# Performance work log

Hardware: AMD Instinct MI355X
Metric: run time of the kernel (lower is better)

## Reference

```python
import jax, jax.numpy as jnp
import numpy as np

B, L, D = 1, 2048, 512
NL, N, K = 4, 16, 4
DI = 2 * D          # mamba expand=2
R = D // 16         # dt_rank = ceil(D/16)
H = 4 * D           # mlp hidden


def _ln(x, w, b, eps=1e-5):
    mu = x.mean(-1, keepdims=True)
    v = ((x - mu) ** 2).mean(-1, keepdims=True)
    return (x - mu) * jax.lax.rsqrt(v + eps) * w + b


def _rms(x, w, eps=1e-5):
    return x * jax.lax.rsqrt((x * x).mean(-1, keepdims=True) + eps) * w


def _ssm_scan(delta, Bm, Cm, u, A, Dp):
    # delta,u: (B,L,DI); Bm,Cm: (B,L,N); A: (DI,N); Dp: (DI,)
    def step(h, inp):
        d_t, b_t, c_t, u_t = inp                              # (B,DI),(B,N),(B,N),(B,DI)
        dA = jnp.exp(d_t[..., None] * A)                      # (B,DI,N)
        h = dA * h + (d_t * u_t)[..., None] * b_t[:, None, :]
        y = jnp.einsum('bdn,bn->bd', h, c_t)
        return h, y
    h0 = jnp.zeros((delta.shape[0], DI, N), delta.dtype)
    xs = (delta.swapaxes(0, 1), Bm.swapaxes(0, 1), Cm.swapaxes(0, 1), u.swapaxes(0, 1))
    _, ys = jax.lax.scan(step, h0, xs)
    return ys.swapaxes(0, 1) + u * Dp


def _mamba(h, in_w, cw, cb, xw, dtw, dtb, A_log, Dp, ow):
    xz = h @ in_w.T                                           # (B,L,2*DI)
    x, z = jnp.split(xz, 2, axis=-1)
    # causal depthwise conv1d, kernel K, left pad K-1
    xp = jnp.pad(x, ((0, 0), (K - 1, 0), (0, 0)))
    Ls = x.shape[1]
    x = sum(cw[:, k] * xp[:, k:k + Ls, :] for k in range(K)) + cb
    x = jax.nn.silu(x)
    dbc = x @ xw.T                                            # (B,L,R+2N)
    dt, Bm, Cm = dbc[..., :R], dbc[..., R:R + N], dbc[..., R + N:]
    delta = jax.nn.softplus(dt @ dtw.T + dtb)                 # (B,L,DI)
    A = -jnp.exp(A_log)                                       # (DI,N)
    y = _ssm_scan(delta, Bm, Cm, x, A, Dp)
    y = y * jax.nn.silu(z)
    return y @ ow.T


def _forward(hidden_states, ln1_w, ln1_b, in_proj_w, conv_w, conv_b, x_proj_w,
             dt_proj_w, dt_proj_b, A_log, D_param, out_proj_w, block_norm_w,
             norm_f_w, ln2_w, ln2_b, fc1_w, fc1_b, fc2_w, fc2_b):
    shortcut = hidden_states
    h = _ln(hidden_states, ln1_w, ln1_b)
    residual = None
    for i in range(in_proj_w.shape[0]):
        residual = h if residual is None else h + residual    # residual_in_fp32
        hn = _rms(residual, block_norm_w[i])                  # fused_add_norm prenorm
        h = _mamba(hn, in_proj_w[i], conv_w[i], conv_b[i], x_proj_w[i],
                   dt_proj_w[i], dt_proj_b[i], A_log[i], D_param[i], out_proj_w[i])
    h = _rms(h + residual, norm_f_w)                          # final rms_norm_fn
    h = shortcut + h
    x = _ln(h, ln2_w, ln2_b)
    x = jax.nn.gelu(x @ fc1_w.T + fc1_b)
    x = x @ fc2_w.T + fc2_b
    return h + x


def setup_inputs() -> dict:
    key = jax.random.key(0)
    ks = jax.random.split(key, 9)
    s = 0.02
    return {
        'hidden_states': jax.random.normal(ks[0], (B, L, D), jnp.float32),
        'ln1_w': jnp.ones((D,), jnp.float32),
        'ln1_b': jnp.zeros((D,), jnp.float32),
        'in_proj_w': jax.random.normal(ks[1], (NL, 2 * DI, D), jnp.float32) * s,
        'conv_w': jax.random.normal(ks[2], (NL, DI, K), jnp.float32) * 0.3,
        'conv_b': jnp.zeros((NL, DI), jnp.float32),
        'x_proj_w': jax.random.normal(ks[3], (NL, R + 2 * N, DI), jnp.float32) * s,
        'dt_proj_w': jax.random.normal(ks[4], (NL, DI, R), jnp.float32) * s,
        'dt_proj_b': jax.random.uniform(ks[5], (NL, DI), jnp.float32, -4.0, -2.0),
        'A_log': jnp.tile(jnp.log(jnp.arange(1, N + 1, dtype=jnp.float32)), (NL, DI, 1)),
        'D_param': jnp.ones((NL, DI), jnp.float32),
        'out_proj_w': jax.random.normal(ks[6], (NL, D, DI), jnp.float32) * s,
        'block_norm_w': jnp.ones((NL, D), jnp.float32),
        'norm_f_w': jnp.ones((D,), jnp.float32),
        'ln2_w': jnp.ones((D,), jnp.float32),
        'ln2_b': jnp.zeros((D,), jnp.float32),
        'fc1_w': jax.random.normal(ks[7], (H, D), jnp.float32) * s,
        'fc1_b': jnp.zeros((H,), jnp.float32),
        'fc2_w': jax.random.normal(ks[8], (D, H), jnp.float32) * s,
        'fc2_b': jnp.zeros((D,), jnp.float32),
    }


def reference(hidden_states, ln1_w, ln1_b, in_proj_w, conv_w, conv_b, x_proj_w,
              dt_proj_w, dt_proj_b, A_log, D_param, out_proj_w, block_norm_w,
              norm_f_w, ln2_w, ln2_b, fc1_w, fc1_b, fc2_w, fc2_b):
    return _forward(hidden_states, ln1_w, ln1_b, in_proj_w, conv_w, conv_b,
                    x_proj_w, dt_proj_w, dt_proj_b, A_log, D_param, out_proj_w,
                    block_norm_w, norm_f_w, ln2_w, ln2_b, fc1_w, fc1_b, fc2_w, fc2_b)
```

## Files before the change

kernel.cpp:

```cpp
#include <hip/hip_runtime.h>
#include <hip/hip_bf16.h>
#include <math.h>

#define L_SEQ 2048
#define Dm    512
#define DI    1024
#define Nst   16
#define Kc    4
#define Rr    32
#define NL    4
#define CH    128
#define LC    (L_SEQ / CH)
#define KSX   8

typedef __attribute__((ext_vector_type(8))) short bf16x8;
typedef __attribute__((ext_vector_type(4))) float f32x4;

__device__ __forceinline__ float act_softplus(float x) {
    return fmaxf(x, 0.f) + log1pf(__expf(-fabsf(x)));
}
__device__ __forceinline__ float act_gelu(float x) {
    float c = 0.7978845608028654f * (x + 0.044715f * x * x * x);
    float t = 1.f - 2.f / (__expf(2.f * c) + 1.f);
    return 0.5f * x * (1.f + t);
}
__device__ __forceinline__ float silu_(float x) {
    return x / (1.f + __expf(-x));
}
__device__ __forceinline__ ushort f2bf(float f) {
    union { float f; unsigned u; } c; c.f = f;
    unsigned r = c.u + 0x7fffu + ((c.u >> 16) & 1u);
    return (ushort)(r >> 16);
}
__device__ __forceinline__ float bf2f(ushort u) {
    union { unsigned u; float f; } c; c.u = ((unsigned)u) << 16;
    return c.f;
}
__device__ __forceinline__ float wave_sum(float v) {
    #pragma unroll
    for (int off = 32; off; off >>= 1) v += __shfl_xor(v, off);
    return v;
}

__global__ __launch_bounds__(256) void setup_kernel(
    const float* __restrict__ s0, ushort* __restrict__ d0, int n0,
    const float* __restrict__ s1, ushort* __restrict__ d1, int n1,
    const float* __restrict__ s2, ushort* __restrict__ d2, int n2,
    const float* __restrict__ s3, ushort* __restrict__ d3, int n3,
    const float* __restrict__ s4, ushort* __restrict__ d4, int n4_,
    const float* __restrict__ s5, ushort* __restrict__ d5, int n5,
    const float* __restrict__ x, const float* __restrict__ w,
    const float* __restrict__ b, const float* __restrict__ rw,
    float* __restrict__ res, ushort* __restrict__ hn_bf)
{
    if (blockIdx.x < 512) {
        int lane = threadIdx.x & 63, wv = threadIdx.x >> 6;
        int row = blockIdx.x * 4 + wv;
        size_t base = (size_t)row * Dm + lane * 8;
        float v[8];
        *(float4*)(v)     = *(const float4*)(x + base);
        *(float4*)(v + 4) = *(const float4*)(x + base + 4);
        float s = 0.f, ss = 0.f;
        #pragma unroll
        for (int q = 0; q < 8; ++q) { s += v[q]; ss += v[q] * v[q]; }
        s = wave_sum(s); ss = wave_sum(ss);
        float mu = s * (1.f / Dm);
        float rs = rsqrtf(ss * (1.f / Dm) - mu * mu + 1e-5f);
        float wv8[8], bv8[8], rv8[8];
        *(float4*)(wv8)     = *(const float4*)(w + lane * 8);
        *(float4*)(wv8 + 4) = *(const float4*)(w + lane * 8 + 4);
        *(float4*)(bv8)     = *(const float4*)(b + lane * 8);
        *(float4*)(bv8 + 4) = *(const float4*)(b + lane * 8 + 4);
        *(float4*)(rv8)     = *(const float4*)(rw + lane * 8);
        *(float4*)(rv8 + 4) = *(const float4*)(rw + lane * 8 + 4);
        float o[8], ss2 = 0.f;
        #pragma unroll
        for (int q = 0; q < 8; ++q) {
            o[q] = (v[q] - mu) * rs * wv8[q] + bv8[q];
            ss2 += o[q] * o[q];
        }
        *(float4*)(res + base)     = *(float4*)(o);
        *(float4*)(res + base + 4) = *(float4*)(o + 4);
        ss2 = wave_sum(ss2);
        float rr = rsqrtf(ss2 * (1.f / Dm) + 1e-5f);
        bf16x8 hb;
        #pragma unroll
        for (int q = 0; q < 8; ++q) hb[q] = (short)f2bf(o[q] * rr * rv8[q]);
        *(bf16x8*)(hn_bf + base) = hb;
        return;
    }
    int i = (blockIdx.x - 512) * 256 + threadIdx.x;
    const float* s; ushort* d;
    if (i < n0) { s = s0; d = d0; }
    else { i -= n0; if (i < n1) { s = s1; d = d1; }
    else { i -= n1; if (i < n2) { s = s2; d = d2; }
    else { i -= n2; if (i < n3) { s = s3; d = d3; }
    else { i -= n3; if (i < n4_) { s = s4; d = d4; }
    else { i -= n4_; if (i < n5) { s = s5; d = d5; } else return; } } } } }
    float4 v = ((const float4*)s)[i];
    ushort4 o;
    o.x = f2bf(v.x); o.y = f2bf(v.y); o.z = f2bf(v.z); o.w = f2bf(v.w);
    ((ushort4*)d)[i] = o;
}

__global__ __launch_bounds__(256) void add_rms_kernel(const ushort* __restrict__ hb,
    float* __restrict__ res, const float* __restrict__ w, ushort* __restrict__ rms_out)
{
    int lane = threadIdx.x & 63, wv = threadIdx.x >> 6;
    int row = blockIdx.x * 4 + wv;
    size_t base = (size_t)row * Dm + lane * 8;
    bf16x8 hv = *(const bf16x8*)(hb + base);
    float v[8];
    *(float4*)(v)     = *(const float4*)(res + base);
    *(float4*)(v + 4) = *(const float4*)(res + base + 4);
    float ss = 0.f;
    #pragma unroll
    for (int q = 0; q < 8; ++q) {
        v[q] += bf2f((ushort)hv[q]);
        ss += v[q] * v[q];
    }
    *(float4*)(res + base)     = *(float4*)(v);
    *(float4*)(res + base + 4) = *(float4*)(v + 4);
    ss = wave_sum(ss);
    float rr = rsqrtf(ss * (1.f / Dm) + 1e-5f);
    float wv8[8];
    *(float4*)(wv8)     = *(const float4*)(w + lane * 8);
    *(float4*)(wv8 + 4) = *(const float4*)(w + lane * 8 + 4);
    bf16x8 ob;
    #pragma unroll
    for (int q = 0; q < 8; ++q) ob[q] = (short)f2bf(v[q] * rr * wv8[q]);
    *(bf16x8*)(rms_out + base) = ob;
}

__global__ __launch_bounds__(256) void final_ln2_kernel(const ushort* __restrict__ hb,
    const float* __restrict__ res, const float* __restrict__ shortcut,
    const float* __restrict__ wf, const float* __restrict__ w2,
    const float* __restrict__ b2, float* __restrict__ hout,
    ushort* __restrict__ yb16)
{
    int lane = threadIdx.x & 63, wv = threadIdx.x >> 6;
    int row = blockIdx.x * 4 + wv;
    size_t base = (size_t)row * Dm + lane * 8;
    bf16x8 hv = *(const bf16x8*)(hb + base);
    float v[8];
    *(float4*)(v)     = *(const float4*)(res + base);
    *(float4*)(v + 4) = *(const float4*)(res + base + 4);
    float ss = 0.f;
    #pragma unroll
    for (int q = 0; q < 8; ++q) {
        v[q] += bf2f((ushort)hv[q]);
        ss += v[q] * v[q];
    }
    ss = wave_sum(ss);
    float rs = rsqrtf(ss * (1.f / Dm) + 1e-5f);
    float sc[8], wf8[8];
    *(float4*)(sc)     = *(const float4*)(shortcut + base);
    *(float4*)(sc + 4) = *(const float4*)(shortcut + base + 4);
    *(float4*)(wf8)     = *(const float4*)(wf + lane * 8);
    *(float4*)(wf8 + 4) = *(const float4*)(wf + lane * 8 + 4);
    float t[8], s2 = 0.f, ss2 = 0.f;
    #pragma unroll
    for (int q = 0; q < 8; ++q) {
        t[q] = sc[q] + v[q] * rs * wf8[q];
        s2 += t[q]; ss2 += t[q] * t[q];
    }
    *(float4*)(hout + base)     = *(float4*)(t);
    *(float4*)(hout + base + 4) = *(float4*)(t + 4);
    s2 = wave_sum(s2); ss2 = wave_sum(ss2);
    float mu = s2 * (1.f / Dm);
    float rsig = rsqrtf(ss2 * (1.f / Dm) - mu * mu + 1e-5f);
    float w28[8], b28[8];
    *(float4*)(w28)     = *(const float4*)(w2 + lane * 8);
    *(float4*)(w28 + 4) = *(const float4*)(w2 + lane * 8 + 4);
    *(float4*)(b28)     = *(const float4*)(b2 + lane * 8);
    *(float4*)(b28 + 4) = *(const float4*)(b2 + lane * 8 + 4);
    bf16x8 ob;
    #pragma unroll
    for (int q = 0; q < 8; ++q) ob[q] = (short)f2bf((t[q] - mu) * rsig * w28[q] + b28[q]);
    *(bf16x8*)(yb16 + base) = ob;
}

template<int BM, int BN, int BK, int EPI>
__global__ __launch_bounds__(256) void gemm_mfma(
    const ushort* __restrict__ A, int lda,
    const ushort* __restrict__ W, int K,
    void* __restrict__ Cout, int ldc,
    const float* __restrict__ bias, const float* __restrict__ addsrc)
{
    constexpr int ROWB  = BK * 2;
    constexpr int SMASK = (ROWB / 16) - 1;
    constexpr int KK    = BK / 32;
    constexpr int WM = BM / 2, WN = BN / 2;
    constexpr int FM = WM / 16, FN = WN / 16;
    constexpr int ISS_A = (BM * ROWB) / 4096;
    constexpr int ISS_W = (BN * ROWB) / 4096;

    __shared__ __align__(16) ushort As[BM * BK];
    __shared__ __align__(16) ushort Ws[BN * BK];

    int tid = threadIdx.x;
    int wave = tid >> 6, lane = tid & 63;
    int wr = wave >> 1, wc = wave & 1;
    int l16 = lane & 15, lk = lane >> 4;
    int bm = blockIdx.y * BM, bn = blockIdx.x * BN;

    const ushort* srcA[ISS_A];
    const ushort* srcW[ISS_W];
    #pragma unroll
    for (int s = 0; s < ISS_A; ++s) {
        int off = s * 4096 + wave * 1024 + lane * 16;
        int row = off / ROWB;
        int slot = (off % ROWB) >> 4;
        int col = ((slot ^ (row & SMASK)) << 3);
        srcA[s] = A + (size_t)(bm + row) * lda + col;
    }
    #pragma unroll
    for (int s = 0; s < ISS_W; ++s) {
        int off = s * 4096 + wave * 1024 + lane * 16;
        int row = off / ROWB;
        int slot = (off % ROWB) >> 4;
        int col = ((slot ^ (row & SMASK)) << 3);
        srcW[s] = W + (size_t)(bn + row) * K + col;
    }
    int aoff[FM][KK], woff[FN][KK];
    #pragma unroll
    for (int i = 0; i < FM; ++i) {
        int row = wr * WM + i * 16 + l16;
        #pragma unroll
        for (int kk = 0; kk < KK; ++kk)
            aoff[i][kk] = row * BK + ((((kk << 2) | lk) ^ (row & SMASK)) << 3);
    }
    #pragma unroll
    for (int j = 0; j < FN; ++j) {
        int row = wc * WN + j * 16 + l16;
        #pragma unroll
        for (int kk = 0; kk < KK; ++kk)
            woff[j][kk] = row * BK + ((((kk << 2) | lk) ^ (row & SMASK)) << 3);
    }

    f32x4 acc[FM][FN] = {};

    for (int k0 = 0; k0 < K; k0 += BK) {
        #pragma unroll
        for (int s = 0; s < ISS_A; ++s)
            __builtin_amdgcn_global_load_lds(
                (const __attribute__((address_space(1))) void*)(srcA[s] + k0),
                (__attribute__((address_space(3))) void*)((char*)As + s * 4096 + wave * 1024),
                16, 0, 0);
        #pragma unroll
        for (int s = 0; s < ISS_W; ++s)
            __builtin_amdgcn_global_load_lds(
                (const __attribute__((address_space(1))) void*)(srcW[s] + k0),
                (__attribute__((address_space(3))) void*)((char*)Ws + s * 4096 + wave * 1024),
                16, 0, 0);
        __syncthreads();
        #pragma unroll
        for (int kk = 0; kk < KK; ++kk) {
            bf16x8 af[FM], wf[FN];
            #pragma unroll
            for (int i = 0; i < FM; ++i) af[i] = *(const bf16x8*)(As + aoff[i][kk]);
            #pragma unroll
            for (int j = 0; j < FN; ++j) wf[j] = *(const bf16x8*)(Ws + woff[j][kk]);
            #pragma unroll
            for (int i = 0; i < FM; ++i)
                #pragma unroll
                for (int j = 0; j < FN; ++j)
                    acc[i][j] = __builtin_amdgcn_mfma_f32_16x16x32_bf16(af[i], wf[j], acc[i][j], 0, 0, 0);
        }
        __syncthreads();
    }

    int orow0 = bm + wr * WM, ocol0 = bn + wc * WN;
    #pragma unroll
    for (int j = 0; j < FN; ++j) {
        int col = ocol0 + j * 16 + l16;
        float bj = 0.f;
        if constexpr (EPI == 2 || EPI == 4) bj = bias[col];
        #pragma unroll
        for (int i = 0; i < FM; ++i) {
            #pragma unroll
            for (int r = 0; r < 4; ++r) {
                int row = orow0 + i * 16 + lk * 4 + r;
                float v = acc[i][j][r];
                if constexpr (EPI == 1) {
                    ((ushort*)Cout)[(size_t)row * ldc + col] = f2bf(v);
                } else if constexpr (EPI == 2) {
                    ((ushort*)Cout)[(size_t)row * ldc + col] = f2bf(act_gelu(v + bj));
                } else if constexpr (EPI == 4) {
                    ((float*)Cout)[(size_t)row * ldc + col] = v + bj + addsrc[(size_t)row * ldc + col];
                }
            }
        }
    }
}

__global__ __launch_bounds__(256) void xproj_conv_kernel(
    const ushort* __restrict__ xz, const float* __restrict__ cw,
    const float* __restrict__ cb, const ushort* __restrict__ W,
    ushort* __restrict__ xc, float* __restrict__ part)
{
    constexpr int BM = 64, BN = 64, BK = 64;
    constexpr int ROWB  = BK * 2;
    constexpr int SMASK = (ROWB / 16) - 1;
    constexpr int KK    = BK / 32;
    constexpr int WM = 32, WN = 32, FM = 2, FN = 2;

    __shared__ __align__(16) ushort As[BM * BK];
    __shared__ __align__(16) ushort Ws[BN * BK];

    int tid = threadIdx.x;
    int wave = tid >> 6, lane = tid & 63;
    int wr = wave >> 1, wc = wave & 1;
    int l16 = lane & 15, lk = lane >> 4;
    int bm = blockIdx.y * BM;
    int z = blockIdx.z;
    int kbeg = z * (DI / KSX);

    const ushort* srcW[2];
    #pragma unroll
    for (int s = 0; s < 2; ++s) {
        int off = s * 4096 + wave * 1024 + lane * 16;
        int row = off / ROWB;
        int slot = (off % ROWB) >> 4;
        int col = ((slot ^ (row & SMASK)) << 3);
        srcW[s] = W + (size_t)row * DI + kbeg + col;
    }
    int aoff[FM][KK], woff[FN][KK];
    #pragma unroll
    for (int i = 0; i < FM; ++i) {
        int row = wr * WM + i * 16 + l16;
        #pragma unroll
        for (int kk = 0; kk < KK; ++kk)
            aoff[i][kk] = row * BK + ((((kk << 2) | lk) ^ (row & SMASK)) << 3);
    }
    #pragma unroll
    for (int j = 0; j < FN; ++j) {
        int row = wc * WN + j * 16 + l16;
        #pragma unroll
        for (int kk = 0; kk < KK; ++kk)
            woff[j][kk] = row * BK + ((((kk << 2) | lk) ^ (row & SMASK)) << 3);
    }

    f32x4 acc[FM][FN] = {};

    for (int k0 = 0; k0 < DI / KSX; k0 += BK) {
        #pragma unroll
        for (int s = 0; s < 2; ++s)
            __builtin_amdgcn_global_load_lds(
                (const __attribute__((address_space(1))) void*)(srcW[s] + k0),
                (__attribute__((address_space(3))) void*)((char*)Ws + s * 4096 + wave * 1024),
                16, 0, 0);
        #pragma unroll
        for (int s = 0; s < 2; ++s) {
            int off = s * 4096 + wave * 1024 + lane * 16;
            int row = off >> 7;
            int slot = (off >> 4) & 7;
            int t = bm + row;
            int dcol = kbeg + k0 + slot * 8;
            float a[8];
            float4 c4[8];
            #pragma unroll
            for (int q = 0; q < 8; ++q) {
                a[q] = cb[dcol + q];
                c4[q] = *(const float4*)(cw + (size_t)(dcol + q) * 4);
            }
            #pragma unroll
            for (int k = 0; k < 4; ++k) {
                int tt = t + k - 3;
                if (tt >= 0) {
                    bf16x8 xv = *(const bf16x8*)(xz + (size_t)tt * (2 * DI) + dcol);
                    #pragma unroll
                    for (int q = 0; q < 8; ++q) {
                        float wk = (k == 0) ? c4[q].x : (k == 1) ? c4[q].y
                                 : (k == 2) ? c4[q].z : c4[q].w;
                        a[q] = fmaf(wk, bf2f((ushort)xv[q]), a[q]);
                    }
                }
            }
            bf16x8 o;
            #pragma unroll
            for (int q = 0; q < 8; ++q) o[q] = (short)f2bf(silu_(a[q]));
            *(bf16x8*)(xc + (size_t)t * DI + dcol) = o;
            *(bf16x8*)(As + row * BK + ((slot ^ (row & SMASK)) << 3)) = o;
        }
        __syncthreads();
        #pragma unroll
        for (int kk = 0; kk < KK; ++kk) {
            bf16x8 af[FM], wf[FN];
            #pragma unroll
            for (int i = 0; i < FM; ++i) af[i] = *(const bf16x8*)(As + aoff[i][kk]);
            #pragma unroll
            for (int j = 0; j < FN; ++j) wf[j] = *(const bf16x8*)(Ws + woff[j][kk]);
            #pragma unroll
            for (int i = 0; i < FM; ++i)
                #pragma unroll
                for (int j = 0; j < FN; ++j)
                    acc[i][j] = __builtin_amdgcn_mfma_f32_16x16x32_bf16(af[i], wf[j], acc[i][j], 0, 0, 0);
        }
        __syncthreads();
    }

    float* coutf = part + (size_t)z * L_SEQ * 64;
    int orow0 = bm + wr * WM, ocol0 = wc * WN;
    #pragma unroll
    for (int j = 0; j < FN; ++j) {
        int col = ocol0 + j * 16 + l16;
        #pragma unroll
        for (int i = 0; i < FM; ++i)
            #pragma unroll
            for (int r = 0; r < 4; ++r) {
                int row = orow0 + i * 16 + lk * 4 + r;
                coutf[(size_t)row * 64 + col] = acc[i][j][r];
            }
    }
}

__global__ __launch_bounds__(256) void scan_chunk_kernel(
    const float* __restrict__ part, const ushort* __restrict__ u,
    const ushort* __restrict__ wdt, const float* __restrict__ dtb,
    const float* __restrict__ A_log,
    float* __restrict__ hend, float* __restrict__ aprod,
    ushort* __restrict__ delta_bf)
{
    __shared__ float sdt[LC][32];
    __shared__ float bsm[LC][16];
    int tid = threadIdx.x;
    int c = blockIdx.x;
    int d = blockIdx.y * 256 + tid;
    int t0 = c * LC;
    const int S = L_SEQ * 64;
    for (int i = tid; i < LC * 48; i += 256) {
        int tt = i / 48, cc = i % 48;
        int idx = (t0 + tt) * 64 + cc;
        float s = 0.f;
        #pragma unroll
        for (int p = 0; p < KSX; ++p) s += part[idx + p * S];
        if (cc < 32) sdt[tt][cc] = s; else bsm[tt][cc - 32] = s;
    }
    bf16x8 wd[4];
    #pragma unroll
    for (int p = 0; p < 4; ++p) wd[p] = *(const bf16x8*)(wdt + (size_t)d * 32 + p * 8);
    float bd = dtb[d];
    float A2[16];
    {
        float a[16];
        #pragma unroll
        for (int q = 0; q < 4; ++q)
            *(float4*)(a + q * 4) = ((const float4*)(A_log + (size_t)d * 16))[q];
        #pragma unroll
        for (int n = 0; n < 16; ++n)
            A2[n] = -__expf(a[n]) * 1.44269504f;
    }
    float h[16], ap[16];
    #pragma unroll
    for (int n = 0; n < 16; ++n) { h[n] = 0.f; ap[n] = 1.f; }
    __syncthreads();
    for (int tt = 0; tt < LC; ++tt) {
        int t = t0 + tt;
        float dtv = bd;
        #pragma unroll
        for (int p = 0; p < 4; ++p)
            #pragma unroll
            for (int e = 0; e < 8; ++e)
                dtv = fmaf(sdt[tt][p * 8 + e], bf2f((ushort)wd[p][e]), dtv);
        ushort dbf = f2bf(act_softplus(dtv));
        delta_bf[(size_t)t * DI + d] = dbf;
        float dt_ = bf2f(dbf);
        float du = dt_ * bf2f(u[(size_t)t * DI + d]);
        #pragma unroll
        for (int n = 0; n < 16; ++n) {
            float dA = exp2f(dt_ * A2[n]);
            h[n] = fmaf(dA, h[n], du * bsm[tt][n]);
            ap[n] *= dA;
        }
    }
    size_t base = ((size_t)c * DI + d) * 16;
    #pragma unroll
    for (int q = 0; q < 4; ++q) {
        ((float4*)(hend + base))[q]  = *(float4*)(h + q * 4);
        ((float4*)(aprod + base))[q] = *(float4*)(ap + q * 4);
    }
}

__global__ __launch_bounds__(64) void chunk_prefix_kernel(
    const float* __restrict__ hend, float* __restrict__ aprod_hin)
{
    int j = blockIdx.x * 64 + threadIdx.x;
    float h = 0.f;
    for (int cg = 0; cg < CH; cg += 8) {
        float ap[8], he[8];
        #pragma unroll
        for (int q = 0; q < 8; ++q) {
            size_t o = (size_t)(cg + q) * (DI * Nst) + j;
            ap[q] = aprod_hin[o]; he[q] = hend[o];
        }
        #pragma unroll
        for (int q = 0; q < 8; ++q) {
            size_t o = (size_t)(cg + q) * (DI * Nst) + j;
            aprod_hin[o] = h;
            h = fmaf(ap[q], h, he[q]);
        }
    }
}

__global__ __launch_bounds__(256) void scan_apply_kernel(
    const float* __restrict__ part, const ushort* __restrict__ delta,
    const ushort* __restrict__ u, const float* __restrict__ A_log,
    const float* __restrict__ Dp, const ushort* __restrict__ xz,
    const float* __restrict__ hin, ushort* __restrict__ y)
{
    __shared__ float bsm[LC][16], csm[LC][16];
    int tid = threadIdx.x;
    int c = blockIdx.x;
    int d = blockIdx.y * 256 + tid;
    int t0 = c * LC;
    const int S = L_SEQ * 64;
    for (int i = tid; i < LC * 32; i += 256) {
        int tt = i >> 5, k = i & 31;
        int idx = (t0 + tt) * 64 + 32 + k;
        float s = 0.f;
        #pragma unroll
        for (int p = 0; p < KSX; ++p) s += part[idx + p * S];
        if (k < 16) bsm[tt][k] = s; else csm[tt][k - 16] = s;
    }
    float A2[16];
    {
        float a[16];
        #pragma unroll
        for (int q = 0; q < 4; ++q)
            *(float4*)(a + q * 4) = ((const float4*)(A_log + (size_t)d * 16))[q];
        #pragma unroll
        for (int n = 0; n < 16; ++n)
            A2[n] = -__expf(a[n]) * 1.44269504f;
    }
    float h[16];
    size_t base = ((size_t)c * DI + d) * 16;
    #pragma unroll
    for (int q = 0; q < 4; ++q)
        *(float4*)(h + q * 4) = ((const float4*)(hin + base))[q];
    float Dval = Dp[d];
    __syncthreads();
    for (int tt = 0; tt < LC; ++tt) {
        int t = t0 + tt;
        float dt_ = bf2f(delta[(size_t)t * DI + d]);
        float u_  = bf2f(u[(size_t)t * DI + d]);
        float du  = dt_ * u_;
        float acc = 0.f;
        #pragma unroll
        for (int n = 0; n < 16; ++n) {
            float dA = exp2f(dt_ * A2[n]);
            h[n] = fmaf(dA, h[n], du * bsm[tt][n]);
            acc = fmaf(h[n], csm[tt][n], acc);
        }
        float zv = bf2f(xz[(size_t)t * (2 * DI) + DI + d]);
        y[(size_t)t * DI + d] = f2bf((acc + u_ * Dval) * silu_(zv));
    }
}

extern "C" void kernel_launch(void* const* d_in, const int* in_sizes, int n_in,
                              void* d_out, int out_size, void* d_ws, size_t ws_size,
                              hipStream_t stream)
{
    const float* hidden     = (const float*)d_in[0];
    const float* ln1_w      = (const float*)d_in[1];
    const float* ln1_b      = (const float*)d_in[2];
    const float* in_proj_w  = (const float*)d_in[3];
    const float* conv_w     = (const float*)d_in[4];
    const float* conv_b     = (const float*)d_in[5];
    const float* x_proj_w   = (const float*)d_in[6];
    const float* dt_proj_w  = (const float*)d_in[7];
    const float* dt_proj_b  = (const float*)d_in[8];
    const float* A_log      = (const float*)d_in[9];
    const float* D_param    = (const float*)d_in[10];
    const float* out_proj_w = (const float*)d_in[11];
    const float* block_norm_w = (const float*)d_in[12];
    const float* norm_f_w   = (const float*)d_in[13];
    const float* ln2_w      = (const float*)d_in[14];
    const float* ln2_b      = (const float*)d_in[15];
    const float* fc1_w      = (const float*)d_in[16];
    const float* fc1_b      = (const float*)d_in[17];
    const float* fc2_w      = (const float*)d_in[18];
    const float* fc2_b      = (const float*)d_in[19];

    char* P = (char*)d_ws;
    auto alloc = [&](size_t bytes) { char* r = P; P += (bytes + 255) & ~(size_t)255; return r; };
    float* hout   = (float*)alloc((size_t)L_SEQ * Dm * 4);
    float* res    = (float*)alloc((size_t)L_SEQ * Dm * 4);
    float* part   = (float*)alloc((size_t)KSX * L_SEQ * 64 * 4);
    float* hend   = (float*)alloc((size_t)CH * DI * Nst * 4);
    float* aprod  = (float*)alloc((size_t)CH * DI * Nst * 4);
    ushort* h_bf  = (ushort*)alloc((size_t)L_SEQ * Dm * 2);
    ushort* delta_bf = (ushort*)alloc((size_t)L_SEQ * DI * 2);
    ushort* hn_bf = (ushort*)alloc((size_t)L_SEQ * Dm * 2);
    ushort* xz_bf = (ushort*)alloc((size_t)L_SEQ * 2 * DI * 2);
    ushort* xc_bf = (ushort*)alloc((size_t)L_SEQ * DI * 2);
    ushort* yb_bf = (ushort*)alloc((size_t)L_SEQ * DI * 2);
    ushort* w_in  = (ushort*)alloc((size_t)NL * 2 * DI * Dm * 2);
    ushort* w_out = (ushort*)alloc((size_t)NL * Dm * DI * 2);
    ushort* w_x   = (ushort*)alloc((size_t)NL * 64 * DI * 2);
    ushort* w_dt  = (ushort*)alloc((size_t)NL * DI * Rr * 2);
    ushort* w_fc1 = (ushort*)alloc((size_t)(4 * Dm) * Dm * 2);
    ushort* w_fc2 = (ushort*)alloc((size_t)Dm * (4 * Dm) * 2);
    float* out  = (float*)d_out;

    {
        int n0 = NL * 2 * DI * Dm / 4, n1 = NL * Dm * DI / 4, n2 = NL * 64 * DI / 4;
        int n3 = NL * DI * Rr / 4, n4_ = 4 * Dm * Dm / 4, n5 = Dm * 4 * Dm / 4;
        int tot = n0 + n1 + n2 + n3 + n4_ + n5;
        int grid = 512 + (tot + 255) / 256;
        setup_kernel<<<grid, 256, 0, stream>>>(
            in_proj_w, w_in, n0, out_proj_w, w_out, n1, x_proj_w, w_x, n2,
            dt_proj_w, w_dt, n3, fc1_w, w_fc1, n4_, fc2_w, w_fc2, n5,
            hidden, ln1_w, ln1_b, block_norm_w, res, hn_bf);
    }

    dim3 gscan(CH, DI / 256);
    for (int i = 0; i < NL; ++i) {
        if (i) add_rms_kernel<<<L_SEQ / 4, 256, 0, stream>>>(h_bf, res,
                                                  block_norm_w + i * Dm, hn_bf);
        gemm_mfma<128, 64, 128, 1><<<dim3(2 * DI / 64, L_SEQ / 128), 256, 0, stream>>>(
            hn_bf, Dm, w_in + (size_t)i * 2 * DI * Dm, Dm, xz_bf, 2 * DI, nullptr, nullptr);
        xproj_conv_kernel<<<dim3(1, L_SEQ / 64, KSX), 256, 0, stream>>>(
            xz_bf, conv_w + i * DI * Kc, conv_b + i * DI,
            w_x + (size_t)i * 64 * DI, xc_bf, part);
        scan_chunk_kernel<<<gscan, 256, 0, stream>>>(part, xc_bf,
                                        w_dt + (size_t)i * DI * Rr, dt_proj_b + i * DI,
                                        A_log + (size_t)i * DI * Nst, hend, aprod, delta_bf);
        chunk_prefix_kernel<<<(DI * Nst) / 64, 64, 0, stream>>>(hend, aprod);
        scan_apply_kernel<<<gscan, 256, 0, stream>>>(part, delta_bf, xc_bf,
                                        A_log + (size_t)i * DI * Nst,
                                        D_param + i * DI, xz_bf, aprod, yb_bf);
        gemm_mfma<64, 32, 128, 1><<<dim3(Dm / 32, L_SEQ / 64), 256, 0, stream>>>(
            yb_bf, DI, w_out + (size_t)i * Dm * DI, DI, h_bf, Dm, nullptr, nullptr);
    }

    final_ln2_kernel<<<L_SEQ / 4, 256, 0, stream>>>(h_bf, res, hidden, norm_f_w,
                                                ln2_w, ln2_b, hout, hn_bf);
    gemm_mfma<128, 64, 128, 2><<<dim3(2048 / 64, L_SEQ / 128), 256, 0, stream>>>(
        hn_bf, Dm, w_fc1, Dm, xz_bf, 2048, fc1_b, nullptr);
    gemm_mfma<64, 32, 128, 4><<<dim3(Dm / 32, L_SEQ / 64), 256, 0, stream>>>(
        xz_bf, 2048, w_fc2, 2048, out, Dm, fc2_b, hout);
}
```

Measured before the change: 390.5 us.

## Fuse residual add and RMSNorm into out_proj epilogue and in_proj prologue

Removes the per-layer add_rms kernel. The out_proj GEMM now adds its fp32 result straight into the residual and writes per-block row sum-of-squares partials. The in_proj GEMM then applies RMSNorm while loading A tiles from the fp32 residual. This also drops the bf16 intermediate h buffer, halves the scan chunk count (CH 128→64), and vectorises chunk_prefix with float4. In exchange, the A tile is now loaded with plain fp32 global loads rather than async LDS loads, and rounding changes slightly because the residual add is done in fp32 instead of via a bf16 intermediate.

```diff
diff --git a/kernel.cpp b/kernel.cpp
--- a/kernel.cpp
+++ b/kernel.cpp
@@ -9,9 +9,10 @@
 #define Kc    4
 #define Rr    32
 #define NL    4
-#define CH    128
+#define CH    64
 #define LC    (L_SEQ / CH)
 #define KSX   8
+#define NXB   16
 
 typedef __attribute__((ext_vector_type(8))) short bf16x8;
 typedef __attribute__((ext_vector_type(4))) float f32x4;
@@ -50,8 +51,8 @@
     const float* __restrict__ s4, ushort* __restrict__ d4, int n4_,
     const float* __restrict__ s5, ushort* __restrict__ d5, int n5,
     const float* __restrict__ x, const float* __restrict__ w,
-    const float* __restrict__ b, const float* __restrict__ rw,
-    float* __restrict__ res, ushort* __restrict__ hn_bf)
+    const float* __restrict__ b,
+    float* __restrict__ res, float* __restrict__ ssp)
 {
     if (blockIdx.x < 512) {
         int lane = threadIdx.x & 63, wv = threadIdx.x >> 6;
@@ -66,13 +67,11 @@
         s = wave_sum(s); ss = wave_sum(ss);
         float mu = s * (1.f / Dm);
         float rs = rsqrtf(ss * (1.f / Dm) - mu * mu + 1e-5f);
-        float wv8[8], bv8[8], rv8[8];
+        float wv8[8], bv8[8];
         *(float4*)(wv8)     = *(const float4*)(w + lane * 8);
         *(float4*)(wv8 + 4) = *(const float4*)(w + lane * 8 + 4);
         *(float4*)(bv8)     = *(const float4*)(b + lane * 8);
         *(float4*)(bv8 + 4) = *(const float4*)(b + lane * 8 + 4);
-        *(float4*)(rv8)     = *(const float4*)(rw + lane * 8);
-        *(float4*)(rv8 + 4) = *(const float4*)(rw + lane * 8 + 4);
         float o[8], ss2 = 0.f;
         #pragma unroll
         for (int q = 0; q < 8; ++q) {
@@ -82,11 +81,8 @@
         *(float4*)(res + base)     = *(float4*)(o);
         *(float4*)(res + base + 4) = *(float4*)(o + 4);
         ss2 = wave_sum(ss2);
-        float rr = rsqrtf(ss2 * (1.f / Dm) + 1e-5f);
-        bf16x8 hb;
-        #pragma unroll
-        for (int q = 0; q < 8; ++q) hb[q] = (short)f2bf(o[q] * rr * rv8[q]);
-        *(bf16x8*)(hn_bf + base) = hb;
+        if (lane < NXB)
+            ssp[(size_t)lane * L_SEQ + row] = (lane == 0) ? ss2 : 0.f;
         return;
     }
     int i = (blockIdx.x - 512) * 256 + threadIdx.x;
@@ -103,54 +99,21 @@
     ((ushort4*)d)[i] = o;
 }
 
-__global__ __launch_bounds__(256) void add_rms_kernel(const ushort* __restrict__ hb,
-    float* __restrict__ res, const float* __restrict__ w, ushort* __restrict__ rms_out)
+__global__ __launch_bounds__(256) void final_ln2_kernel(const float* __restrict__ res,
+    const float* __restrict__ shortcut,
+    const float* __restrict__ wf, const float* __restrict__ w2,
+    const float* __restrict__ b2, float* __restrict__ hout,
+    ushort* __restrict__ yb16)
 {
     int lane = threadIdx.x & 63, wv = threadIdx.x >> 6;
     int row = blockIdx.x * 4 + wv;
     size_t base = (size_t)row * Dm + lane * 8;
-    bf16x8 hv = *(const bf16x8*)(hb + base);
     float v[8];
     *(float4*)(v)     = *(const float4*)(res + base);
     *(float4*)(v + 4) = *(const float4*)(res + base + 4);
     float ss = 0.f;
     #pragma unroll
-    for (int q = 0; q < 8; ++q) {
-        v[q] += bf2f((ushort)hv[q]);
-        ss += v[q] * v[q];
-    }
-    *(float4*)(res + base)     = *(float4*)(v);
-    *(float4*)(res + base + 4) = *(float4*)(v + 4);
-    ss = wave_sum(ss);
-    float rr = rsqrtf(ss * (1.f / Dm) + 1e-5f);
-    float wv8[8];
-    *(float4*)(wv8)     = *(const float4*)(w + lane * 8);
-    *(float4*)(wv8 + 4) = *(const float4*)(w + lane * 8 + 4);
-    bf16x8 ob;
-    #pragma unroll
-    for (int q = 0; q < 8; ++q) ob[q] = (short)f2bf(v[q] * rr * wv8[q]);
-    *(bf16x8*)(rms_out + base) = ob;
-}
-
-__global__ __launch_bounds__(256) void final_ln2_kernel(const ushort* __restrict__ hb,
-    const float* __restrict__ res, const float* __restrict__ shortcut,
-    const float* __restrict__ wf, const float* __restrict__ w2,
-    const float* __restrict__ b2, float* __restrict__ hout,
-    ushort* __restrict__ yb16)
-{
-    int lane = threadIdx.x & 63, wv = threadIdx.x >> 6;
-    int row = blockIdx.x * 4 + wv;
-    size_t base = (size_t)row * Dm + lane * 8;
-    bf16x8 hv = *(const bf16x8*)(hb + base);
-    float v[8];
-    *(float4*)(v)     = *(const float4*)(res + base);
-    *(float4*)(v + 4) = *(const float4*)(res + base + 4);
-    float ss = 0.f;
-    #pragma unroll
-    for (int q = 0; q < 8; ++q) {
-        v[q] += bf2f((ushort)hv[q]);
-        ss += v[q] * v[q];
-    }
+    for (int q = 0; q < 8; ++q) ss += v[q] * v[q];
     ss = wave_sum(ss);
     float rs = rsqrtf(ss * (1.f / Dm) + 1e-5f);
     float sc[8], wf8[8];
@@ -185,7 +148,8 @@
     const ushort* __restrict__ A, int lda,
     const ushort* __restrict__ W, int K,
     void* __restrict__ Cout, int ldc,
-    const float* __restrict__ bias, const float* __restrict__ addsrc)
+    const float* __restrict__ bias, const float* __restrict__ addsrc,
+    float* __restrict__ ssp)
 {
     constexpr int ROWB  = BK * 2;
     constexpr int SMASK = (ROWB / 16) - 1;
@@ -197,6 +161,7 @@
 
     __shared__ __align__(16) ushort As[BM * BK];
     __shared__ __align__(16) ushort Ws[BN * BK];
+    __shared__ float ss_lds[2][BM];
 
     int tid = threadIdx.x;
     int wave = tid >> 6, lane = tid & 63;
@@ -288,9 +253,138 @@
                     ((ushort*)Cout)[(size_t)row * ldc + col] = f2bf(act_gelu(v + bj));
                 } else if constexpr (EPI == 4) {
                     ((float*)Cout)[(size_t)row * ldc + col] = v + bj + addsrc[(size_t)row * ldc + col];
+                } else if constexpr (EPI == 5) {
+                    size_t idx = (size_t)row * ldc + col;
+                    float nv = ((float*)Cout)[idx] + v;
+                    ((float*)Cout)[idx] = nv;
+                    float sq = nv * nv;
+                    sq += __shfl_xor(sq, 1);
+                    sq += __shfl_xor(sq, 2);
+                    sq += __shfl_xor(sq, 4);
+                    sq += __shfl_xor(sq, 8);
+                    if (l16 == 0)
+                        ss_lds[wc][wr * WM + i * 16 + lk * 4 + r] = sq;
                 }
             }
         }
+    }
+    if constexpr (EPI == 5) {
+        __syncthreads();
+        if (tid < BM)
+            ssp[(size_t)blockIdx.x * L_SEQ + bm + tid] = ss_lds[0][tid] + ss_lds[1][tid];
+    }
+}
+
+__global__ __launch_bounds__(256) void gemm_rms_kernel(
+    const float* __restrict__ res, const float* __restrict__ ssp,
+    const float* __restrict__ bw, const ushort* __restrict__ W,
+    ushort* __restrict__ Cout)
+{
+    constexpr int BM = 128, BN = 64, BK = 128, K = Dm;
+    constexpr int ROWB  = BK * 2;
+    constexpr int SMASK = 15;
+    constexpr int KK    = 4;
+    constexpr int WM = 64, WN = 32, FM = 4, FN = 2;
+    constexpr int ISS_A = 8, ISS_W = 4;
+
+    __shared__ __align__(16) ushort As[BM * BK];
+    __shared__ __align__(16) ushort Ws[BN * BK];
+    __shared__ float rr_lds[BM];
+
+    int tid = threadIdx.x;
+    int wave = tid >> 6, lane = tid & 63;
+    int wr = wave >> 1, wc = wave & 1;
+    int l16 = lane & 15, lk = lane >> 4;
+    int bm = blockIdx.y * BM, bn = blockIdx.x * BN;
+
+    if (tid < BM) {
+        int row = bm + tid;
+        float s = 0.f;
+        #pragma unroll
+        for (int x = 0; x < NXB; ++x) s += ssp[(size_t)x * L_SEQ + row];
+        rr_lds[tid] = rsqrtf(s * (1.f / Dm) + 1e-5f);
+    }
+
+    const ushort* srcW[ISS_W];
+    #pragma unroll
+    for (int s = 0; s < ISS_W; ++s) {
+        int off = s * 4096 + wave * 1024 + lane * 16;
+        int row = off / ROWB;
+        int slot = (off % ROWB) >> 4;
+        int col = ((slot ^ (row & SMASK)) << 3);
+        srcW[s] = W + (size_t)(bn + row) * K + col;
+    }
+    int aoff[FM][KK], woff[FN][KK];
+    #pragma unroll
+    for (int i = 0; i < FM; ++i) {
+        int row = wr * WM + i * 16 + l16;
+        #pragma unroll
+        for (int kk = 0; kk < KK; ++kk)
+            aoff[i][kk] = row * BK + ((((kk << 2) | lk) ^ (row & SMASK)) << 3);
+    }
+    #pragma unroll
+    for (int j = 0; j < FN; ++j) {
+        int row = wc * WN + j * 16 + l16;
+        #pragma unroll
+        for (int kk = 0; kk < KK; ++kk)
+            woff[j][kk] = row * BK + ((((kk << 2) | lk) ^ (row & SMASK)) << 3);
+    }
+    __syncthreads();
+
+    f32x4 acc[FM][FN] = {};
+
+    for (int k0 = 0; k0 < K; k0 += BK) {
+        #pragma unroll
+        for (int s = 0; s < ISS_W; ++s)
+            __builtin_amdgcn_global_load_lds(
+                (const __attribute__((address_space(1))) void*)(srcW[s] + k0),
+                (__attribute__((address_space(3))) void*)((char*)Ws + s * 4096 + wave * 1024),
+                16, 0, 0);
+        #pragma unroll
+        for (int s = 0; s < ISS_A; ++s) {
+            int off = s * 4096 + wave * 1024 + lane * 16;
+            int row = off >> 8;
+            int slot = (off >> 4) & 15;
+            int k = k0 + slot * 8;
+            float rv[8], bw8[8];
+            *(float4*)(rv)     = *(const float4*)(res + (size_t)(bm + row) * Dm + k);
+            *(float4*)(rv + 4) = *(const float4*)(res + (size_t)(bm + row) * Dm + k + 4);
+            *(float4*)(bw8)     = *(const float4*)(bw + k);
+            *(float4*)(bw8 + 4) = *(const float4*)(bw + k + 4);
+            float rr = rr_lds[row];
+            bf16x8 o;
+            #pragma unroll
+            for (int q = 0; q < 8; ++q) o[q] = (short)f2bf(rv[q] * rr * bw8[q]);
+            *(bf16x8*)(As + row * BK + ((slot ^ (row & SMASK)) << 3)) = o;
+        }
+        __syncthreads();
+        #pragma unroll
+        for (int kk = 0; kk < KK; ++kk) {
+            bf16x8 af[FM], wf[FN];
+            #pragma unroll
+            for (int i = 0; i < FM; ++i) af[i] = *(const bf16x8*)(As + aoff[i][kk]);
+            #pragma unroll
+            for (int j = 0; j < FN; ++j) wf[j] = *(const bf16x8*)(Ws + woff[j][kk]);
+            #pragma unroll
+            for (int i = 0; i < FM; ++i)
+                #pragma unroll
+                for (int j = 0; j < FN; ++j)
+                    acc[i][j] = __builtin_amdgcn_mfma_f32_16x16x32_bf16(af[i], wf[j], acc[i][j], 0, 0, 0);
+        }
+        __syncthreads();
+    }
+
+    int orow0 = bm + wr * WM, ocol0 = bn + wc * WN;
+    #pragma unroll
+    for (int j = 0; j < FN; ++j) {
+        int col = ocol0 + j * 16 + l16;
+        #pragma unroll
+        for (int i = 0; i < FM; ++i)
+            #pragma unroll
+            for (int r = 0; r < 4; ++r) {
+                int row = orow0 + i * 16 + lk * 4 + r;
+                Cout[(size_t)row * (2 * DI) + col] = f2bf(acc[i][j][r]);
+            }
     }
 }
 
@@ -485,20 +579,24 @@
 __global__ __launch_bounds__(64) void chunk_prefix_kernel(
     const float* __restrict__ hend, float* __restrict__ aprod_hin)
 {
-    int j = blockIdx.x * 64 + threadIdx.x;
-    float h = 0.f;
+    int j4 = (blockIdx.x * 64 + threadIdx.x) * 4;
+    float4 h = { 0.f, 0.f, 0.f, 0.f };
     for (int cg = 0; cg < CH; cg += 8) {
-        float ap[8], he[8];
+        float4 ap[8], he[8];
         #pragma unroll
         for (int q = 0; q < 8; ++q) {
-            size_t o = (size_t)(cg + q) * (DI * Nst) + j;
-            ap[q] = aprod_hin[o]; he[q] = hend[o];
+            size_t o = (size_t)(cg + q) * (DI * Nst) + j4;
+            ap[q] = *(const float4*)(aprod_hin + o);
+            he[q] = *(const float4*)(hend + o);
         }
         #pragma unroll
         for (int q = 0; q < 8; ++q) {
-            size_t o = (size_t)(cg + q) * (DI * Nst) + j;
-            aprod_hin[o] = h;
-            h = fmaf(ap[q], h, he[q]);
+            size_t o = (size_t)(cg + q) * (DI * Nst) + j4;
+            *(float4*)(aprod_hin + o) = h;
+            h.x = fmaf(ap[q].x, h.x, he[q].x);
+            h.y = fmaf(ap[q].y, h.y, he[q].y);
+            h.z = fmaf(ap[q].z, h.z, he[q].z);
+            h.w = fmaf(ap[q].w, h.w, he[q].w);
         }
     }
 }
@@ -586,10 +684,10 @@
     auto alloc = [&](size_t bytes) { char* r = P; P += (bytes + 255) & ~(size_t)255; return r; };
     float* hout   = (float*)alloc((size_t)L_SEQ * Dm * 4);
     float* res    = (float*)alloc((size_t)L_SEQ * Dm * 4);
+    float* ssp    = (float*)alloc((size_t)NXB * L_SEQ * 4);
     float* part   = (float*)alloc((size_t)KSX * L_SEQ * 64 * 4);
     float* hend   = (float*)alloc((size_t)CH * DI * Nst * 4);
     float* aprod  = (float*)alloc((size_t)CH * DI * Nst * 4);
-    ushort* h_bf  = (ushort*)alloc((size_t)L_SEQ * Dm * 2);
     ushort* delta_bf = (ushort*)alloc((size_t)L_SEQ * DI * 2);
     ushort* hn_bf = (ushort*)alloc((size_t)L_SEQ * Dm * 2);
     ushort* xz_bf = (ushort*)alloc((size_t)L_SEQ * 2 * DI * 2);
@@ -611,33 +709,31 @@
         setup_kernel<<<grid, 256, 0, stream>>>(
             in_proj_w, w_in, n0, out_proj_w, w_out, n1, x_proj_w, w_x, n2,
             dt_proj_w, w_dt, n3, fc1_w, w_fc1, n4_, fc2_w, w_fc2, n5,
-            hidden, ln1_w, ln1_b, block_norm_w, res, hn_bf);
+            hidden, ln1_w, ln1_b, res, ssp);
     }
 
     dim3 gscan(CH, DI / 256);
     for (int i = 0; i < NL; ++i) {
-        if (i) add_rms_kernel<<<L_SEQ / 4, 256, 0, stream>>>(h_bf, res,
-                                                  block_norm_w + i * Dm, hn_bf);
-        gemm_mfma<128, 64, 128, 1><<<dim3(2 * DI / 64, L_SEQ / 128), 256, 0, stream>>>(
-            hn_bf, Dm, w_in + (size_t)i * 2 * DI * Dm, Dm, xz_bf, 2 * DI, nullptr, nullptr);
+        gemm_rms_kernel<<<dim3(2 * DI / 64, L_SEQ / 128), 256, 0, stream>>>(
+            res, ssp, block_norm_w + i * Dm, w_in + (size_t)i * 2 * DI * Dm, xz_bf);
         xproj_conv_kernel<<<dim3(1, L_SEQ / 64, KSX), 256, 0, stream>>>(
             xz_bf, conv_w + i * DI * Kc, conv_b + i * DI,
             w_x + (size_t)i * 64 * DI, xc_bf, part);
         scan_chunk_kernel<<<gscan, 256, 0, stream>>>(part, xc_bf,
                                         w_dt + (size_t)i * DI * Rr, dt_proj_b + i * DI,
                                         A_log + (size_t)i * DI * Nst, hend, aprod, delta_bf);
-        chunk_prefix_kernel<<<(DI * Nst) / 64, 64, 0, stream>>>(hend, aprod);
+        chunk_prefix_kernel<<<(DI * Nst) / 256, 64, 0, stream>>>(hend, aprod);
         scan_apply_kernel<<<gscan, 256, 0, stream>>>(part, delta_bf, xc_bf,
                                         A_log + (size_t)i * DI * Nst,
                                         D_param + i * DI, xz_bf, aprod, yb_bf);
-        gemm_mfma<64, 32, 128, 1><<<dim3(Dm / 32, L_SEQ / 64), 256, 0, stream>>>(
-            yb_bf, DI, w_out + (size_t)i * Dm * DI, DI, h_bf, Dm, nullptr, nullptr);
-    }
-
-    final_ln2_kernel<<<L_SEQ / 4, 256, 0, stream>>>(h_bf, res, hidden, norm_f_w,
+        gemm_mfma<64, 32, 128, 5><<<dim3(Dm / 32, L_SEQ / 64), 256, 0, stream>>>(
+            yb_bf, DI, w_out + (size_t)i * Dm * DI, DI, res, Dm, nullptr, nullptr, ssp);
+    }
+
+    final_ln2_kernel<<<L_SEQ / 4, 256, 0, stream>>>(res, hidden, norm_f_w,
                                                 ln2_w, ln2_b, hout, hn_bf);
     gemm_mfma<128, 64, 128, 2><<<dim3(2048 / 64, L_SEQ / 128), 256, 0, stream>>>(
-        hn_bf, Dm, w_fc1, Dm, xz_bf, 2048, fc1_b, nullptr);
+        hn_bf, Dm, w_fc1, Dm, xz_bf, 2048, fc1_b, nullptr, nullptr);
     gemm_mfma<64, 32, 128, 4><<<dim3(Dm / 32, L_SEQ / 64), 256, 0, stream>>>(
-        xz_bf, 2048, w_fc2, 2048, out, Dm, fc2_b, hout);
-}
+        xz_bf, 2048, w_fc2, 2048, out, Dm, fc2_b, hout, nullptr);
+}
```

Result: slower. 479.6 us (+22.8%).
